# Kernel optimization log

Measured on AMD Instinct MI355X. Metric: run time of the kernel, lower is better.

## Reference

```python
import jax, jax.numpy as jnp
import numpy as np

E = 1024
H = 16
D = E // H
FF = 4096
EPS = 1e-5


def _layernorm(x, gamma, beta):
    mu = jnp.mean(x, axis=-1, keepdims=True)
    var = jnp.var(x, axis=-1, keepdims=True)
    return (x - mu) * jax.lax.rsqrt(var + EPS) * gamma + beta


def setup_inputs() -> dict:
    key = jax.random.key(0)
    ks = jax.random.split(key, 12)
    B, C = 4, 2048
    s_e = 1.0 / np.sqrt(E)
    s_f = 1.0 / np.sqrt(FF)
    return {
        "x": jax.random.normal(ks[0], (B, C, E), dtype=jnp.float32),
        "ln1_g": jnp.ones((E,), jnp.float32),
        "ln1_b": jnp.zeros((E,), jnp.float32),
        "Wq": jax.random.normal(ks[1], (E, H * D), jnp.float32) * s_e,
        "Wk": jax.random.normal(ks[2], (E, H * D), jnp.float32) * s_e,
        "Wv": jax.random.normal(ks[3], (E, H * D), jnp.float32) * s_e,
        "Wo": jax.random.normal(ks[4], (H * D, E), jnp.float32) * s_e,
        "ln2_g": jnp.ones((E,), jnp.float32),
        "ln2_b": jnp.zeros((E,), jnp.float32),
        "W1": jax.random.normal(ks[5], (E, FF), jnp.float32) * s_e,
        "b1": jnp.zeros((FF,), jnp.float32),
        "W2": jax.random.normal(ks[6], (FF, E), jnp.float32) * s_f,
        "b2": jnp.zeros((E,), jnp.float32),
    }


def reference(x, ln1_g, ln1_b, Wq, Wk, Wv, Wo, ln2_g, ln2_b, W1, b1, W2, b2):
    B, C, _ = x.shape

    # --- pre-LN causal self-attention ---
    h = _layernorm(x, ln1_g, ln1_b)
    Q = (h @ Wq).reshape(B, C, H, D).transpose(0, 2, 1, 3)  # [B,H,C,D]
    K = (h @ Wk).reshape(B, C, H, D).transpose(0, 2, 1, 3)
    V = (h @ Wv).reshape(B, C, H, D).transpose(0, 2, 1, 3)

    scores = jnp.einsum("bhqd,bhkd->bhqk", Q, K) / jnp.sqrt(jnp.float32(D))
    causal = jnp.tril(jnp.ones((C, C), dtype=bool))
    scores = jnp.where(causal, scores, -jnp.inf)
    weights = jax.nn.softmax(scores, axis=-1)  # dropout omitted (eval)
    hidden = jnp.einsum("bhqk,bhkd->bhqd", weights, V)
    hidden = hidden.transpose(0, 2, 1, 3).reshape(B, C, H * D)
    x = x + hidden @ Wo

    # --- FFN ---
    h2 = _layernorm(x, ln2_g, ln2_b)
    h2 = jax.nn.gelu(h2 @ W1 + b1, approximate=False)
    x = x + (h2 @ W2 + b2)
    return x
```

## Files before the change

### kernel.cpp

```cpp
#include <hip/hip_runtime.h>

typedef __bf16 bf16x8 __attribute__((ext_vector_type(8)));
typedef float f32x4 __attribute__((ext_vector_type(4)));
typedef unsigned short u16x8 __attribute__((ext_vector_type(8)));
typedef unsigned short u16x4 __attribute__((ext_vector_type(4)));

__device__ __forceinline__ unsigned short f2bf(float f) {
    return __builtin_bit_cast(unsigned short, (__bf16)f);
}

__device__ __forceinline__ float fexp2(float x) {
#if __has_builtin(__builtin_amdgcn_exp2f)
    return __builtin_amdgcn_exp2f(x);
#else
    float r; asm("v_exp_f32 %0, %1\n\ts_nop 1" : "=v"(r) : "v"(x)); return r;
#endif
}

__device__ __forceinline__ void gload_lds16(const unsigned short* g, unsigned short* l) {
    __builtin_amdgcn_global_load_lds(
        (const __attribute__((address_space(1))) unsigned int*)g,
        (__attribute__((address_space(3))) unsigned int*)l, 16, 0, 0);
}

#define VMW(n) asm volatile("s_waitcnt vmcnt(" #n ")" ::: "memory")
#define SBAR() __builtin_amdgcn_s_barrier()
#define SCHED0() __builtin_amdgcn_sched_barrier(0)

#define QSCALE 0.18033688011112042f

__global__ __launch_bounds__(256) void ln_kernel(
    const float* __restrict__ x, const float* __restrict__ g,
    const float* __restrict__ b, unsigned short* __restrict__ out)
{
    const int row = blockIdx.x;
    const int tid = threadIdx.x;
    const float4 v = reinterpret_cast<const float4*>(x + (size_t)row * 1024)[tid];
    float s = v.x + v.y + v.z + v.w;
    float q = v.x * v.x + v.y * v.y + v.z * v.z + v.w * v.w;
#pragma unroll
    for (int off = 32; off >= 1; off >>= 1) {
        s += __shfl_xor(s, off);
        q += __shfl_xor(q, off);
    }
    __shared__ float ss[4], sq[4];
    const int wid = tid >> 6, lane = tid & 63;
    if (lane == 0) { ss[wid] = s; sq[wid] = q; }
    __syncthreads();
    s = ss[0] + ss[1] + ss[2] + ss[3];
    q = sq[0] + sq[1] + sq[2] + sq[3];
    const float mu = s * (1.0f / 1024.0f);
    const float var = q * (1.0f / 1024.0f) - mu * mu;
    const float rs = rsqrtf(var + 1e-5f);
    const float4 gv = reinterpret_cast<const float4*>(g)[tid];
    const float4 bv = reinterpret_cast<const float4*>(b)[tid];
    u16x4 o;
    o[0] = f2bf((v.x - mu) * rs * gv.x + bv.x);
    o[1] = f2bf((v.y - mu) * rs * gv.y + bv.y);
    o[2] = f2bf((v.z - mu) * rs * gv.z + bv.z);
    o[3] = f2bf((v.w - mu) * rs * gv.w + bv.w);
    reinterpret_cast<u16x4*>(out + (size_t)row * 1024)[tid] = o;
}

__global__ __launch_bounds__(256) void convT_kernel(
    const float* __restrict__ W, unsigned short* __restrict__ Wt, int K, int N)
{
    __shared__ float t[32][33];
    const int n0 = blockIdx.x * 32, k0 = blockIdx.y * 32;
    const int tx = threadIdx.x & 31;
    const int ty = threadIdx.x >> 5;
#pragma unroll
    for (int i = 0; i < 4; i++)
        t[ty + 8 * i][tx] = W[(size_t)(k0 + ty + 8 * i) * N + (n0 + tx)];
    __syncthreads();
#pragma unroll
    for (int i = 0; i < 4; i++)
        Wt[(size_t)(n0 + ty + 8 * i) * K + (k0 + tx)] = f2bf(t[tx][ty + 8 * i]);
}

__global__ __launch_bounds__(256) void convT4_kernel(
    const float* __restrict__ A0, const float* __restrict__ A1,
    const float* __restrict__ A2, const float* __restrict__ A3,
    unsigned short* __restrict__ Wt)
{
    constexpr int E = 1024;
    const int z = blockIdx.z;
    const float* W = (z == 0) ? A0 : (z == 1) ? A1 : (z == 2) ? A2 : A3;
    unsigned short* dst = Wt + (size_t)z * E * E;
    __shared__ float t[32][33];
    const int n0 = blockIdx.x * 32, k0 = blockIdx.y * 32;
    const int tx = threadIdx.x & 31;
    const int ty = threadIdx.x >> 5;
#pragma unroll
    for (int i = 0; i < 4; i++)
        t[ty + 8 * i][tx] = W[(size_t)(k0 + ty + 8 * i) * E + (n0 + tx)];
    __syncthreads();
#pragma unroll
    for (int i = 0; i < 4; i++)
        dst[(size_t)(n0 + ty + 8 * i) * E + (k0 + tx)] = f2bf(t[tx][ty + 8 * i]);
}

__global__ __launch_bounds__(256) void gemm128_kernel(
    const unsigned short* __restrict__ A, const unsigned short* __restrict__ Bt,
    const float* __restrict__ resid, float* __restrict__ out, int M, int N, int K)
{
    __shared__ unsigned short Al[128][64];
    __shared__ unsigned short Bl[128][64];
    const int tid = threadIdx.x;
    const int lane = tid & 63, wid = tid >> 6;
    const int wr = wid >> 1, wc = wid & 1;
    const int li = lane & 15, lg = lane >> 4;
    const int m0 = blockIdx.y * 128, n0 = blockIdx.x * 128;
    const int srow = lane >> 3;
    const int schunk = ((lane & 7) ^ srow) * 8;
    const unsigned short* Asrc = A + (size_t)(m0 + wid * 32 + srow) * K + schunk;
    const unsigned short* Bsrc = Bt + (size_t)(n0 + wid * 32 + srow) * K + schunk;
    f32x4 acc[4][4] = {};

    for (int k0 = 0; k0 < K; k0 += 64) {
        __syncthreads();
#pragma unroll
        for (int i = 0; i < 4; i++) {
            gload_lds16(Asrc + k0 + (size_t)i * 8 * K, &Al[wid * 32 + i * 8][0]);
            gload_lds16(Bsrc + k0 + (size_t)i * 8 * K, &Bl[wid * 32 + i * 8][0]);
        }
        __syncthreads();
#pragma unroll
        for (int ks = 0; ks < 2; ks++) {
            bf16x8 af[4], bfr[4];
#pragma unroll
            for (int m = 0; m < 4; m++)
                af[m] = *reinterpret_cast<const bf16x8*>(
                    &Al[wr * 64 + m * 16 + li][((ks * 4 + lg) ^ (li & 7)) * 8]);
#pragma unroll
            for (int n = 0; n < 4; n++)
                bfr[n] = *reinterpret_cast<const bf16x8*>(
                    &Bl[wc * 64 + n * 16 + li][((ks * 4 + lg) ^ (li & 7)) * 8]);
#pragma unroll
            for (int m = 0; m < 4; m++)
#pragma unroll
                for (int n = 0; n < 4; n++)
                    acc[m][n] = __builtin_amdgcn_mfma_f32_16x16x32_bf16(af[m], bfr[n], acc[m][n], 0, 0, 0);
        }
    }

#pragma unroll
    for (int m = 0; m < 4; m++)
#pragma unroll
        for (int r = 0; r < 4; r++) {
            const int row = m0 + wr * 64 + m * 16 + lg * 4 + r;
#pragma unroll
            for (int n = 0; n < 4; n++) {
                const int col = n0 + wc * 64 + n * 16 + li;
                out[(size_t)row * N + col] = acc[m][n][r] + resid[(size_t)row * N + col];
            }
        }
}

template <int EPI, int SPLITK>
__global__ __launch_bounds__(512, 2) void gemm256_kernel(
    const unsigned short* __restrict__ A, const unsigned short* __restrict__ Bt,
    const float* __restrict__ bias, void* __restrict__ out, int M, int N, int K)
{
    __shared__ __align__(16) unsigned short Al[2][256][64];
    __shared__ __align__(16) unsigned short Bl[2][256][64];
    const int tid = threadIdx.x;
    const int lane = tid & 63, wid = tid >> 6;
    const int wr = wid >> 2, wc = wid & 3;
    const int li = lane & 15, lg = lane >> 4;

    const int nblk = (M >> 8) * (N >> 8);
    const int cpx = gridDim.x >> 3;
    const int swz = ((int)blockIdx.x & 7) * cpx + ((int)blockIdx.x >> 3);
    int tsw = swz, sid = 0;
    if (SPLITK == 2) { sid = (swz >= nblk) ? 1 : 0; tsw = swz - sid * nblk; }
    const int nx = N >> 8;
    const int bx = tsw % nx, by = tsw / nx;
    const int m0 = by * 256, n0 = bx * 256;
    const int kOff = (SPLITK == 2) ? sid * (K >> 1) : 0;
    const int kLen = (SPLITK == 2) ? (K >> 1) : K;

    const int srow = lane >> 3;
    const int sgc = ((lane & 7) ^ srow) * 8;
    const unsigned short* aSrc = A + (size_t)(m0 + wid * 16 + srow) * K + kOff + sgc;
    const unsigned short* bSrc = Bt + (size_t)(n0 + wid * 16 + srow) * K + kOff + sgc;
    unsigned short* aDst = &Al[0][wid * 16][0];
    unsigned short* bDst = &Bl[0][wid * 16][0];

    auto stA = [&](int u, int h) {
        const unsigned short* s = aSrc + (size_t)(h * 128) * K + u * 64;
        unsigned short* d = aDst + (u & 1) * (256 * 64) + h * 128 * 64;
        gload_lds16(s, d);
        gload_lds16(s + (size_t)8 * K, d + 8 * 64);
    };
    auto stB = [&](int u, int h) {
        const unsigned short* s = bSrc + (size_t)(h * 128) * K + u * 64;
        unsigned short* d = bDst + (u & 1) * (256 * 64) + h * 128 * 64;
        gload_lds16(s, d);
        gload_lds16(s + (size_t)8 * K, d + 8 * 64);
    };

    f32x4 acc[8][4] = {};
    bf16x8 af[8], bn0[4], bn1[4];

    auto ldA = [&](int buf, int mh) {
#pragma unroll
        for (int m = 0; m < 4; m++)
#pragma unroll
            for (int ks = 0; ks < 2; ks++)
                af[m * 2 + ks] = *reinterpret_cast<const bf16x8*>(
                    &Al[buf][wr * 128 + mh * 64 + m * 16 + li][((ks * 4 + lg) ^ (li & 7)) * 8]);
    };
    auto ldB = [&](bf16x8* dst, int buf, int nh) {
#pragma unroll
        for (int n = 0; n < 2; n++)
#pragma unroll
            for (int ks = 0; ks < 2; ks++)
                dst[n * 2 + ks] = *reinterpret_cast<const bf16x8*>(
                    &Bl[buf][wc * 64 + nh * 32 + n * 16 + li][((ks * 4 + lg) ^ (li & 7)) * 8]);
    };
    auto quad = [&](const bf16x8* bfr, int mh, int nh) {
        __builtin_amdgcn_s_setprio(1);
#pragma unroll
        for (int ks = 0; ks < 2; ks++)
#pragma unroll
            for (int m = 0; m < 4; m++)
#pragma unroll
                for (int n = 0; n < 2; n++)
                    acc[mh * 4 + m][nh * 2 + n] = __builtin_amdgcn_mfma_f32_16x16x32_bf16(
                        af[m * 2 + ks], bfr[n * 2 + ks], acc[mh * 4 + m][nh * 2 + n], 0, 0, 0);
        __builtin_amdgcn_s_setprio(0);
    };

    const int NI = kLen >> 7;

    stA(0, 0); stA(0, 1); stB(0, 0); stB(0, 1);
    stB(1, 0); stB(1, 1);
    VMW(4);
    SBAR(); SCHED0();

    for (int I = 0; I < NI; ++I) {
        const int u0 = 2 * I;
        const bool hn = (I + 1 < NI);
        ldA(0, 0); ldB(bn0, 0, 0);
        stA(u0 + 1, 0);
        SBAR(); SCHED0();
        quad(bn0, 0, 0);
        SBAR(); SCHED0();
        ldB(bn1, 0, 1);
        stA(u0 + 1, 1);
        SBAR(); SCHED0();
        quad(bn1, 0, 1);
        SBAR(); SCHED0();
        ldA(0, 1);
        if (hn) stB(u0 + 2, 0);
        SBAR(); SCHED0();
        quad(bn1, 1, 1);
        SBAR(); SCHED0();
        if (hn) stB(u0 + 2, 1);
        SBAR(); SCHED0();
        quad(bn0, 1, 0);
        if (hn) { VMW(4); } else { VMW(0); }
        SBAR(); SCHED0();
        ldA(1, 0); ldB(bn0, 1, 0);
        if (hn) stA(u0 + 2, 0);
        SBAR(); SCHED0();
        quad(bn0, 0, 0);
        SBAR(); SCHED0();
        ldB(bn1, 1, 1);
        if (hn) stA(u0 + 2, 1);
        SBAR(); SCHED0();
        quad(bn1, 0, 1);
        SBAR(); SCHED0();
        ldA(1, 1);
        if (hn) stB(u0 + 3, 0);
        SBAR(); SCHED0();
        quad(bn1, 1, 1);
        SBAR(); SCHED0();
        if (hn) stB(u0 + 3, 1);
        SBAR(); SCHED0();
        quad(bn0, 1, 0);
        if (hn) { VMW(4); } else { VMW(0); }
        SBAR(); SCHED0();
    }

#pragma unroll
    for (int ma = 0; ma < 8; ma++) {
#pragma unroll
        for (int r = 0; r < 4; r++) {
            const int row = m0 + wr * 128 + ma * 16 + lg * 4 + r;
#pragma unroll
            for (int n = 0; n < 4; n++) {
                const int col = n0 + wc * 64 + n * 16 + li;
                float v = acc[ma][n][r];
                if constexpr (EPI == 2) {
                    v += bias[col];
                    float a2 = 1.5957691216f * (v + 0.044715f * v * v * v);
                    a2 = fminf(a2, 80.0f);
                    const float t = __expf(a2);
                    v = v * t * __builtin_amdgcn_rcpf(t + 1.0f);
                    reinterpret_cast<unsigned short*>(out)[(size_t)row * N + col] = f2bf(v);
                } else if constexpr (EPI == 4) {
                    float* op = reinterpret_cast<float*>(out) + (size_t)sid * M * N;
                    op[(size_t)row * N + col] = v;
                } else {
                    const float sc = (col < 1024) ? QSCALE : 1.0f;
                    reinterpret_cast<unsigned short*>(out)[(size_t)row * N + col] = f2bf(v * sc);
                }
            }
        }
    }
}

__global__ __launch_bounds__(256) void w2red_kernel(
    const float* __restrict__ p0, const float* __restrict__ p1,
    const float* __restrict__ x1, const float* __restrict__ b2,
    float* __restrict__ out)
{
    const int i = blockIdx.x * 256 + threadIdx.x;
    const float4 a = reinterpret_cast<const float4*>(p0)[i];
    const float4 b = reinterpret_cast<const float4*>(p1)[i];
    const float4 r = reinterpret_cast<const float4*>(x1)[i];
    const float4 bb = reinterpret_cast<const float4*>(b2)[i & 255];
    float4 o;
    o.x = a.x + b.x + r.x + bb.x;
    o.y = a.y + b.y + r.y + bb.y;
    o.z = a.z + b.z + r.z + bb.z;
    o.w = a.w + b.w + r.w + bb.w;
    reinterpret_cast<float4*>(out)[i] = o;
}

__global__ __launch_bounds__(256, 4) void flash_kernel(
    const unsigned short* __restrict__ QKV, unsigned short* __restrict__ O)
{
    constexpr int C = 2048, HD3 = 3072, HD = 1024, NT = 32;
    __shared__ unsigned short Kl[2][64][64];
    __shared__ unsigned short Vt[2][64][64];
    __shared__ unsigned short Pl[64][64];
    const int tid = threadIdx.x;
    const int lane = tid & 63, wid = tid >> 6;
    const int li = lane & 15, lg = lane >> 4;
    const int flat = blockIdx.x;
    const int bh = flat & 63;
    const int pair = flat >> 6;
    const int b = bh >> 4, h = bh & 15;
    const size_t baseQ = ((size_t)b * C) * HD3 + (size_t)h * 64;
    const size_t baseK = baseQ + 1024;
    const size_t baseV = baseQ + 2048;
    const size_t baseO = ((size_t)b * C) * HD + (size_t)h * 64;

    const int srow = lane >> 3;
    const int sgc = ((lane & 7) ^ srow) * 8;
    const int vx = lane & 7;

    const u16x8 onesu = {0x3F80, 0x3F80, 0x3F80, 0x3F80, 0x3F80, 0x3F80, 0x3F80, 0x3F80};
    const bf16x8 ones = __builtin_bit_cast(bf16x8, onesu);

    for (int half = 0; half < 2; half++) {
        const int qt = (half == 0) ? pair : (NT - 1 - pair);
        const int q0 = qt * 64;
        const int qrow = q0 + wid * 16 + li;
        const bf16x8 qa0 = *reinterpret_cast<const bf16x8*>(&QKV[baseQ + (size_t)qrow * HD3 + lg * 8]);
        const bf16x8 qa1 = *reinterpret_cast<const bf16x8*>(&QKV[baseQ + (size_t)qrow * HD3 + 32 + lg * 8]);
        const int myrow0 = q0 + wid * 16 + lg * 4;

        f32x4 acc[4] = {};
        f32x4 accl = {};
        int cur = 0;

        auto stage = [&](int k0s, int buf) {
#pragma unroll
            for (int i = 0; i < 2; i++)
                gload_lds16(&QKV[baseK + (size_t)(k0s + wid * 16 + i * 8 + srow) * HD3 + sgc],
                            &Kl[buf][wid * 16 + i * 8][0]);
#pragma unroll
            for (int i = 0; i < 2; i++) {
                const int lkey = 8 * wid + srow + 32 * i;
                const u16x8 vv = *reinterpret_cast<const u16x8*>(
                    &QKV[baseV + (size_t)(k0s + lkey) * HD3 + vx * 8]);
                const int vc = wid + 4 * i;
#pragma unroll
                for (int j = 0; j < 8; j++)
                    Vt[buf][vx * 8 + j][((vc ^ j ^ vx) & 7) * 8 + srow] = vv[j];
            }
        };

        __syncthreads();
        stage(0, 0);
        __syncthreads();

        auto tile_body = [&](int t, bool diag, bool pre) {
            const int k0 = t * 64;
            u16x8 vr0, vr1;
            if (pre) {
                const int kn = k0 + 64;
#pragma unroll
                for (int i = 0; i < 2; i++)
                    gload_lds16(&QKV[baseK + (size_t)(kn + wid * 16 + i * 8 + srow) * HD3 + sgc],
                                &Kl[cur ^ 1][wid * 16 + i * 8][0]);
                vr0 = *reinterpret_cast<const u16x8*>(
                    &QKV[baseV + (size_t)(kn + 8 * wid + srow) * HD3 + vx * 8]);
                vr1 = *reinterpret_cast<const u16x8*>(
                    &QKV[baseV + (size_t)(kn + 8 * wid + srow + 32) * HD3 + vx * 8]);
            }

            f32x4 s[4] = {};
            __builtin_amdgcn_s_setprio(1);
#pragma unroll
            for (int n = 0; n < 4; n++) {
                const int row = n * 16 + li;
                const bf16x8 kb0 = *reinterpret_cast<const bf16x8*>(
                    &Kl[cur][row][(lg ^ (li & 7)) * 8]);
                const bf16x8 kb1 = *reinterpret_cast<const bf16x8*>(
                    &Kl[cur][row][((4 + lg) ^ (li & 7)) * 8]);
                s[n] = __builtin_amdgcn_mfma_f32_16x16x32_bf16(qa0, kb0, s[n], 0, 0, 0);
                s[n] = __builtin_amdgcn_mfma_f32_16x16x32_bf16(qa1, kb1, s[n], 0, 0, 0);
            }
            __builtin_amdgcn_s_setprio(0);

#pragma unroll
            for (int n = 0; n < 4; n++) {
#pragma unroll
                for (int r = 0; r < 4; r++) {
                    float pv = fexp2(s[n][r]);
                    if (diag) {
                        const int key = k0 + n * 16 + li;
                        if (key > myrow0 + r) pv = 0.0f;
                    }
                    Pl[wid * 16 + lg * 4 + r][((2 * n + (li >> 3) + 2 * lg) & 7) * 8 + (li & 7)] = f2bf(pv);
                }
            }

            if (pre) {
#pragma unroll
                for (int j = 0; j < 8; j++)
                    Vt[cur ^ 1][vx * 8 + j][((wid ^ j ^ vx) & 7) * 8 + srow] = vr0[j];
#pragma unroll
                for (int j = 0; j < 8; j++)
                    Vt[cur ^ 1][vx * 8 + j][(((wid + 4) ^ j ^ vx) & 7) * 8 + srow] = vr1[j];
            }

            __builtin_amdgcn_s_setprio(1);
#pragma unroll
            for (int ks = 0; ks < 2; ks++) {
                const bf16x8 pa = *reinterpret_cast<const bf16x8*>(
                    &Pl[wid * 16 + li][((ks * 4 + lg + 2 * (li >> 2)) & 7) * 8]);
#pragma unroll
                for (int n = 0; n < 4; n++) {
                    const int row = n * 16 + li;
                    const bf16x8 vb = *reinterpret_cast<const bf16x8*>(
                        &Vt[cur][row][(((ks * 4 + lg) ^ (row & 7) ^ (row >> 3)) & 7) * 8]);
                    acc[n] = __builtin_amdgcn_mfma_f32_16x16x32_bf16(pa, vb, acc[n], 0, 0, 0);
                }
                accl = __builtin_amdgcn_mfma_f32_16x16x32_bf16(pa, ones, accl, 0, 0, 0);
            }
            __builtin_amdgcn_s_setprio(0);

            __syncthreads();
            cur ^= 1;
        };

        for (int t = 0; t < qt; t++) tile_body(t, false, true);
        tile_body(qt, true, false);

#pragma unroll
        for (int r = 0; r < 4; r++) {
            const float inv = 1.0f / accl[r];
            const int row = myrow0 + r;
#pragma unroll
            for (int n = 0; n < 4; n++)
                O[baseO + (size_t)row * HD + n * 16 + li] = f2bf(acc[n][r] * inv);
        }
    }
}

extern "C" void kernel_launch(void* const* d_in, const int* in_sizes, int n_in,
                              void* d_out, int out_size, void* d_ws, size_t ws_size,
                              hipStream_t stream) {
    constexpr int B = 4, C = 2048, E = 1024, H = 16, FF = 4096;
    constexpr int M = B * C;

    const float* x     = (const float*)d_in[0];
    const float* ln1_g = (const float*)d_in[1];
    const float* ln1_b = (const float*)d_in[2];
    const float* Wq    = (const float*)d_in[3];
    const float* Wk    = (const float*)d_in[4];
    const float* Wv    = (const float*)d_in[5];
    const float* Wo    = (const float*)d_in[6];
    const float* ln2_g = (const float*)d_in[7];
    const float* ln2_b = (const float*)d_in[8];
    const float* W1    = (const float*)d_in[9];
    const float* b1    = (const float*)d_in[10];
    const float* W2    = (const float*)d_in[11];
    const float* b2    = (const float*)d_in[12];

    char* p = (char*)d_ws;
    auto alloc = [&](size_t bytes) { void* r = (void*)p; p += (bytes + 255) & ~(size_t)255; return r; };
    unsigned short* WqT  = (unsigned short*)alloc((size_t)E * E * 2);
    unsigned short* WkT  = (unsigned short*)alloc((size_t)E * E * 2);
    unsigned short* WvT  = (unsigned short*)alloc((size_t)E * E * 2);
    unsigned short* WoT  = (unsigned short*)alloc((size_t)E * E * 2);
    unsigned short* W1T  = (unsigned short*)alloc((size_t)E * FF * 2);
    unsigned short* W2T  = (unsigned short*)alloc((size_t)FF * E * 2);
    unsigned short* hb   = (unsigned short*)alloc((size_t)M * E * 2);
    unsigned short* QKVb = (unsigned short*)alloc((size_t)M * 3 * E * 2);
    unsigned short* attn = (unsigned short*)alloc((size_t)M * E * 2);
    float*          x1   = (float*)alloc((size_t)M * E * 4);
    unsigned short* h2   = (unsigned short*)alloc((size_t)M * E * 2);
    unsigned short* ff   = (unsigned short*)alloc((size_t)M * FF * 2);
    (void)WkT; (void)WvT;
    float* parts = (float*)hb;

    convT4_kernel<<<dim3(E / 32, E / 32, 4), 256, 0, stream>>>(Wq, Wk, Wv, Wo, WqT);
    convT_kernel<<<dim3(FF / 32, E / 32), 256, 0, stream>>>(W1, W1T, E, FF);
    convT_kernel<<<dim3(E / 32, FF / 32), 256, 0, stream>>>(W2, W2T, FF, E);

    ln_kernel<<<M, 256, 0, stream>>>(x, ln1_g, ln1_b, hb);

    gemm256_kernel<5, 1><<<dim3((3 * E / 256) * (M / 256)), 512, 0, stream>>>(
        hb, WqT, nullptr, QKVb, M, 3 * E, E);

    flash_kernel<<<dim3(1024), 256, 0, stream>>>(QKVb, attn);

    gemm128_kernel<<<dim3(E / 128, M / 128), 256, 0, stream>>>(
        attn, WoT, x, x1, M, E, E);

    ln_kernel<<<M, 256, 0, stream>>>(x1, ln2_g, ln2_b, h2);

    gemm256_kernel<2, 1><<<dim3((FF / 256) * (M / 256)), 512, 0, stream>>>(
        h2, W1T, b1, ff, M, FF, E);

    gemm256_kernel<4, 2><<<dim3(2 * (E / 256) * (M / 256)), 512, 0, stream>>>(
        ff, W2T, nullptr, parts, M, E, FF);
    w2red_kernel<<<dim3(M * E / 4 / 256), 256, 0, stream>>>(
        parts, parts + (size_t)M * E, x1, b2, (float*)d_out);
}
```

Baseline: 374.5 us.

## Replace split-K partial buffers and reduce kernel with atomic accumulation into output

The Wo GEMM epilogue now also writes x1 + b2 into the final output, and the split-K W2 GEMM atomically adds its partial sums into that output. This removes the separate reduction kernel and the round trip of two full fp32 partial buffers. It also drops the sched_barrier hints from the 256-tile GEMM main loop, which lets the compiler reorder instructions between barriers. The cost is fp32 atomic traffic to global memory and a summation order that is no longer deterministic.

```diff
diff --git a/kernel.cpp b/kernel.cpp
--- a/kernel.cpp
+++ b/kernel.cpp
@@ -25,7 +25,6 @@
 
 #define VMW(n) asm volatile("s_waitcnt vmcnt(" #n ")" ::: "memory")
 #define SBAR() __builtin_amdgcn_s_barrier()
-#define SCHED0() __builtin_amdgcn_sched_barrier(0)
 
 #define QSCALE 0.18033688011112042f
 
@@ -102,7 +101,8 @@
 
 __global__ __launch_bounds__(256) void gemm128_kernel(
     const unsigned short* __restrict__ A, const unsigned short* __restrict__ Bt,
-    const float* __restrict__ resid, float* __restrict__ out, int M, int N, int K)
+    const float* __restrict__ resid, const float* __restrict__ b2,
+    float* __restrict__ out, float* __restrict__ dinit, int M, int N, int K)
 {
     __shared__ unsigned short Al[128][64];
     __shared__ unsigned short Bl[128][64];
@@ -152,7 +152,9 @@
 #pragma unroll
             for (int n = 0; n < 4; n++) {
                 const int col = n0 + wc * 64 + n * 16 + li;
-                out[(size_t)row * N + col] = acc[m][n][r] + resid[(size_t)row * N + col];
+                const float xv = acc[m][n][r] + resid[(size_t)row * N + col];
+                out[(size_t)row * N + col] = xv;
+                dinit[(size_t)row * N + col] = xv + b2[col];
             }
         }
 }
@@ -237,51 +239,51 @@
     stA(0, 0); stA(0, 1); stB(0, 0); stB(0, 1);
     stB(1, 0); stB(1, 1);
     VMW(4);
-    SBAR(); SCHED0();
+    SBAR();
 
     for (int I = 0; I < NI; ++I) {
         const int u0 = 2 * I;
         const bool hn = (I + 1 < NI);
         ldA(0, 0); ldB(bn0, 0, 0);
         stA(u0 + 1, 0);
-        SBAR(); SCHED0();
+        SBAR();
         quad(bn0, 0, 0);
-        SBAR(); SCHED0();
+        SBAR();
         ldB(bn1, 0, 1);
         stA(u0 + 1, 1);
-        SBAR(); SCHED0();
+        SBAR();
         quad(bn1, 0, 1);
-        SBAR(); SCHED0();
+        SBAR();
         ldA(0, 1);
         if (hn) stB(u0 + 2, 0);
-        SBAR(); SCHED0();
+        SBAR();
         quad(bn1, 1, 1);
-        SBAR(); SCHED0();
+        SBAR();
         if (hn) stB(u0 + 2, 1);
-        SBAR(); SCHED0();
+        SBAR();
         quad(bn0, 1, 0);
         if (hn) { VMW(4); } else { VMW(0); }
-        SBAR(); SCHED0();
+        SBAR();
         ldA(1, 0); ldB(bn0, 1, 0);
         if (hn) stA(u0 + 2, 0);
-        SBAR(); SCHED0();
+        SBAR();
         quad(bn0, 0, 0);
-        SBAR(); SCHED0();
+        SBAR();
         ldB(bn1, 1, 1);
         if (hn) stA(u0 + 2, 1);
-        SBAR(); SCHED0();
+        SBAR();
         quad(bn1, 0, 1);
-        SBAR(); SCHED0();
+        SBAR();
         ldA(1, 1);
         if (hn) stB(u0 + 3, 0);
-        SBAR(); SCHED0();
+        SBAR();
         quad(bn1, 1, 1);
-        SBAR(); SCHED0();
+        SBAR();
         if (hn) stB(u0 + 3, 1);
-        SBAR(); SCHED0();
+        SBAR();
         quad(bn0, 1, 0);
         if (hn) { VMW(4); } else { VMW(0); }
-        SBAR(); SCHED0();
+        SBAR();
     }
 
 #pragma unroll
@@ -300,9 +302,8 @@
                     const float t = __expf(a2);
                     v = v * t * __builtin_amdgcn_rcpf(t + 1.0f);
                     reinterpret_cast<unsigned short*>(out)[(size_t)row * N + col] = f2bf(v);
-                } else if constexpr (EPI == 4) {
-                    float* op = reinterpret_cast<float*>(out) + (size_t)sid * M * N;
-                    op[(size_t)row * N + col] = v;
+                } else if constexpr (EPI == 6) {
+                    atomicAdd(reinterpret_cast<float*>(out) + (size_t)row * N + col, v);
                 } else {
                     const float sc = (col < 1024) ? QSCALE : 1.0f;
                     reinterpret_cast<unsigned short*>(out)[(size_t)row * N + col] = f2bf(v * sc);
@@ -310,24 +311,6 @@
             }
         }
     }
-}
-
-__global__ __launch_bounds__(256) void w2red_kernel(
-    const float* __restrict__ p0, const float* __restrict__ p1,
-    const float* __restrict__ x1, const float* __restrict__ b2,
-    float* __restrict__ out)
-{
-    const int i = blockIdx.x * 256 + threadIdx.x;
-    const float4 a = reinterpret_cast<const float4*>(p0)[i];
-    const float4 b = reinterpret_cast<const float4*>(p1)[i];
-    const float4 r = reinterpret_cast<const float4*>(x1)[i];
-    const float4 bb = reinterpret_cast<const float4*>(b2)[i & 255];
-    float4 o;
-    o.x = a.x + b.x + r.x + bb.x;
-    o.y = a.y + b.y + r.y + bb.y;
-    o.z = a.z + b.z + r.z + bb.z;
-    o.w = a.w + b.w + r.w + bb.w;
-    reinterpret_cast<float4*>(out)[i] = o;
 }
 
 __global__ __launch_bounds__(256, 4) void flash_kernel(
@@ -509,7 +492,6 @@
     unsigned short* h2   = (unsigned short*)alloc((size_t)M * E * 2);
     unsigned short* ff   = (unsigned short*)alloc((size_t)M * FF * 2);
     (void)WkT; (void)WvT;
-    float* parts = (float*)hb;
 
     convT4_kernel<<<dim3(E / 32, E / 32, 4), 256, 0, stream>>>(Wq, Wk, Wv, Wo, WqT);
     convT_kernel<<<dim3(FF / 32, E / 32), 256, 0, stream>>>(W1, W1T, E, FF);
@@ -523,15 +505,13 @@
     flash_kernel<<<dim3(1024), 256, 0, stream>>>(QKVb, attn);
 
     gemm128_kernel<<<dim3(E / 128, M / 128), 256, 0, stream>>>(
-        attn, WoT, x, x1, M, E, E);
+        attn, WoT, x, b2, x1, (float*)d_out, M, E, E);
 
     ln_kernel<<<M, 256, 0, stream>>>(x1, ln2_g, ln2_b, h2);
 
     gemm256_kernel<2, 1><<<dim3((FF / 256) * (M / 256)), 512, 0, stream>>>(
         h2, W1T, b1, ff, M, FF, E);
 
-    gemm256_kernel<4, 2><<<dim3(2 * (E / 256) * (M / 256)), 512, 0, stream>>>(
-        ff, W2T, nullptr, parts, M, E, FF);
-    w2red_kernel<<<dim3(M * E / 4 / 256), 256, 0, stream>>>(
-        parts, parts + (size_t)M * E, x1, b2, (float*)d_out);
-}
+    gemm256_kernel<6, 2><<<dim3(2 * (E / 256) * (M / 256)), 512, 0, stream>>>(
+        ff, W2T, nullptr, (float*)d_out, M, E, FF);
+}
```

Measured after the change: 409.5 us. 1.09x slower.
